# Kernel optimization log

Measured on AMD Instinct MI355X. Metric: run time of the kernel, lower is better.

Reference implementation:

```python
import jax, jax.numpy as jnp
import numpy as np

K = 3        # kernel
S = 2        # downsample scale
P = 1        # padding
C = 96       # input channels
G = C // 6   # groups = 16 (use_group=True)
BN_EPS = 1e-5


def setup_inputs() -> dict:
    key = jax.random.key(0)
    k1, k2, k3, k4, k5 = jax.random.split(key, 5)
    b, h, w = 4, 256, 512
    x = jax.random.normal(k1, (b, C, h, w), dtype=jnp.float32)
    # convbn: Conv2d(C, C*S, k=3, stride=2, pad=1, bias=False) + BatchNorm2d(C*S)
    w1 = jax.random.normal(k2, (C * S, C, K, K), dtype=jnp.float32) * 0.05
    gamma = jax.random.uniform(k3, (C * S,), dtype=jnp.float32, minval=0.5, maxval=1.5)
    beta = jax.random.normal(k4, (C * S,), dtype=jnp.float32) * 0.1
    # 1x1 conv: C*S -> G * K^2, bias=False
    w2 = jax.random.normal(k5, (G * K * K, C * S, 1, 1), dtype=jnp.float32) * 0.05
    return {"x": x, "w1": w1, "gamma": gamma, "beta": beta, "w2": w2}


def _conv(x, w, stride, pad):
    return jax.lax.conv_general_dilated(
        x, w, window_strides=(stride, stride), padding=[(pad, pad), (pad, pad)],
        dimension_numbers=("NCHW", "OIHW", "NCHW"))


def _unfold_patches(x):
    # F.unfold(x, [K,K], stride=S, padding=P) viewed as (b, c, K*K, h', w')
    b, c, h, w = x.shape
    ho, wo = h // S, w // S
    xp = jnp.pad(x, ((0, 0), (0, 0), (P, P), (P, P)))
    taps = [xp[:, :, i:i + ho * S:S, j:j + wo * S:S] for i in range(K) for j in range(K)]
    return jnp.stack(taps, axis=2)  # (b, c, K^2, h', w')


def reference(x, w1, gamma, beta, w2):
    b, c, h, w = x.shape
    ho, wo = h // S, w // S
    # conv_mask branch: conv -> BN (eval: mean=0, var=1) -> LeakyReLU(0.1) -> 1x1 conv
    y = _conv(x, w1, S, P)
    y = y * (gamma / jnp.sqrt(1.0 + BN_EPS))[None, :, None, None] + beta[None, :, None, None]
    y = jnp.where(y >= 0, y, 0.1 * y)
    mask = _conv(y, w2, 1, 0)                                  # (b, G*K^2, h', w')
    mask = mask.reshape(b, 1, G, K * K, ho, wo)
    mask = jax.nn.softmax(mask, axis=3)
    # unfold and group split: channel index = i*G + g  (torch view semantics)
    patches = _unfold_patches(x)                               # (b, c, K^2, h', w')
    patches = patches.reshape(b, c // G, G, K * K, ho, wo)
    out = jnp.sum(mask * patches, axis=3)                      # (b, c//G, G, h', w')
    return out.reshape(b, c, ho, wo)
```

## Files before the change

kernel.cpp:

```cpp
#include <hip/hip_runtime.h>
#include <hip/hip_bf16.h>

#define Bb 4
#define Cc 96
#define Hh 256
#define Ww 512
#define OC 192
#define HO 128
#define WO 256
#define Gg 16
#define CPG 6

typedef __attribute__((ext_vector_type(4))) float f32x4;
typedef __attribute__((ext_vector_type(8))) short bf16x8;
typedef __attribute__((ext_vector_type(4))) short bf16x4;

static __device__ __forceinline__ ushort f2b(float f) {
    __hip_bfloat16 h = __float2bfloat16(f);
    return *reinterpret_cast<ushort*>(&h);
}
static __device__ __forceinline__ float b2f(ushort u) {
    unsigned int v = ((unsigned int)u) << 16;
    return __builtin_bit_cast(float, v);
}

__global__ __launch_bounds__(64) void pack_w1(const float* __restrict__ w1,
                                              ushort* __restrict__ apack) {
    const int blk = blockIdx.x;
    const int k0 = blk / 12;
    const int mf = blk % 12;
    const int lane = threadIdx.x;
    const int m = mf * 16 + (lane & 15);
    const int chunk = k0 / 9;
    const int tap = k0 % 9;
    ushort* dst = apack + (((size_t)(k0 * 12 + mf) * 64) + lane) * 8;
#pragma unroll
    for (int j = 0; j < 8; ++j) {
        const int klocal = ((lane >> 4) << 3) + j;
        const int ic = chunk * 32 + klocal;
        dst[j] = f2b(w1[(size_t)(m * Cc + ic) * 9 + tap]);
    }
}

__global__ __launch_bounds__(64) void pack_w2(const float* __restrict__ w2,
                                              ushort* __restrict__ w2p) {
    const int blk = blockIdx.x;
    const int ks = blk / 9;
    const int mf = blk % 9;
    const int lane = threadIdx.x;
    const int X = lane & 15;
    const int qq = X >> 2;
    const int rr = X & 3;
    const int s = mf * 4 + rr;
    const int g = qq * 4 + s / 9;
    const int k = s % 9;
    const int m = g * 9 + k;
    ushort* dst = w2p + (((size_t)(ks * 9 + mf) * 64) + lane) * 8;
#pragma unroll
    for (int j = 0; j < 8; ++j) {
        const int klocal = ((lane >> 4) << 3) + j;
        const int c = ks * 32 + klocal;
        dst[j] = f2b(w2[(size_t)m * OC + c]);
    }
}

#define XL_MAIN (6 * 4 * 128 * 8)
#define UNION_USHORTS (XL_MAIN + 3 * 32)

__global__ __launch_bounds__(512, 4) void fused(
        const float* __restrict__ x, const ushort* __restrict__ apack,
        const ushort* __restrict__ w2p,
        const float* __restrict__ gamma, const float* __restrict__ beta,
        float* __restrict__ out) {
    __shared__ __align__(16) ushort smem[UNION_USHORTS];
    __shared__ float sc[OC], bi[OC];

    const int bid = blockIdx.x;
    const int owt = bid & 1;
    const int oh = (bid >> 1) & 127;
    const int b = bid >> 8;
    const int ow0 = owt * 128;
    const int tid = threadIdx.x;
    const int wid = tid >> 6;
    const int wm = wid & 1;
    const int wn = wid >> 1;
    const int lane = tid & 63;
    const int r = lane & 15;
    const int q = lane >> 4;

    if (tid < OC) {
        const float bnr = 1.0f / sqrtf(1.0f + 1e-5f);
        sc[tid] = gamma[tid] * bnr;
        bi[tid] = beta[tid];
    }

    f32x4 cacc[6][2];
#pragma unroll
    for (int mf = 0; mf < 6; ++mf)
#pragma unroll
        for (int nf = 0; nf < 2; ++nf) cacc[mf][nf] = (f32x4){0.f, 0.f, 0.f, 0.f};

    const size_t chs = (size_t)Hh * Ww;

    for (int chunk = 0; chunk < 3; ++chunk) {
        __syncthreads();
        const int icc = chunk * 32;
#pragma unroll
        for (int it = 0; it < 3; ++it) {
            const int g2 = tid + (it << 9);
            const int oct = g2 & 3;
            const int colp = (g2 >> 2) & 127;
            const int row = g2 >> 9;
            const int ih = 2 * oh - 1 + row;
            const int gcol = 2 * ow0 + 2 * colp;
            float2 v[8];
            if (ih >= 0) {
                const float* xp = x + ((size_t)(b * Cc + icc + (oct << 3)) * Hh + ih) * Ww + gcol;
#pragma unroll
                for (int j = 0; j < 8; ++j)
                    v[j] = *reinterpret_cast<const float2*>(xp + (size_t)j * chs);
            } else {
#pragma unroll
                for (int j = 0; j < 8; ++j) v[j] = make_float2(0.f, 0.f);
            }
            bf16x8 u0, u1;
#pragma unroll
            for (int j = 0; j < 8; ++j) {
                u0[j] = (short)f2b(v[j].x);
                u1[j] = (short)f2b(v[j].y);
            }
            *reinterpret_cast<bf16x8*>(smem + (((row * 2 + 0) * 4 + oct) * 128 + colp) * 8) = u0;
            *reinterpret_cast<bf16x8*>(smem + (((row * 2 + 1) * 4 + oct) * 128 + colp) * 8) = u1;
        }
        if (tid < 12) {
            const int oct = tid & 3;
            const int row = tid >> 2;
            const int ih = 2 * oh - 1 + row;
            const int gcol = 2 * ow0 - 1;
            float v[8];
            if (ih >= 0 && gcol >= 0) {
                const float* xp = x + ((size_t)(b * Cc + icc + (oct << 3)) * Hh + ih) * Ww + gcol;
#pragma unroll
                for (int j = 0; j < 8; ++j) v[j] = xp[(size_t)j * chs];
            } else {
#pragma unroll
                for (int j = 0; j < 8; ++j) v[j] = 0.f;
            }
            bf16x8 u;
#pragma unroll
            for (int j = 0; j < 8; ++j) u[j] = (short)f2b(v[j]);
            *reinterpret_cast<bf16x8*>(smem + XL_MAIN + row * 32 + oct * 8) = u;
        }
        __syncthreads();

#pragma unroll
        for (int tap = 0; tap < 9; ++tap) {
            const int kh = tap / 3, kw = tap % 3;
            const int par = (kw == 1) ? 0 : 1;
            const int cb = (kw == 0) ? -1 : 0;
            const int k0 = chunk * 9 + tap;

            bf16x8 af[6];
            const ushort* ap = apack + (((size_t)(k0 * 12 + wm * 6) * 64) + lane) * 8;
#pragma unroll
            for (int mf = 0; mf < 6; ++mf)
                af[mf] = *reinterpret_cast<const bf16x8*>(ap + (size_t)mf * 64 * 8);

            bf16x8 bfr[2];
#pragma unroll
            for (int nf = 0; nf < 2; ++nf) {
                const int n = wn * 32 + nf * 16 + r;
                const int colc = n + cb;
                const ushort* src = (colc >= 0)
                    ? smem + (((kh * 2 + par) * 4 + q) * 128 + colc) * 8
                    : smem + XL_MAIN + kh * 32 + q * 8;
                bfr[nf] = *reinterpret_cast<const bf16x8*>(src);
            }
#pragma unroll
            for (int mf = 0; mf < 6; ++mf)
#pragma unroll
                for (int nf = 0; nf < 2; ++nf)
                    cacc[mf][nf] = __builtin_amdgcn_mfma_f32_16x16x32_bf16(
                        af[mf], bfr[nf], cacc[mf][nf], 0, 0, 0);
        }
    }

    __syncthreads();
#pragma unroll
    for (int mf = 0; mf < 6; ++mf) {
        const int cbase = wm * 96 + mf * 16;
        const int coct = (cbase >> 3) + (q >> 1);
#pragma unroll
        for (int nf = 0; nf < 2; ++nf) {
            const int ow = wn * 32 + nf * 16 + r;
            ushort pk[4];
#pragma unroll
            for (int rr = 0; rr < 4; ++rr) {
                const int oc = cbase + q * 4 + rr;
                float v = cacc[mf][nf][rr] * sc[oc] + bi[oc];
                v = (v >= 0.f) ? v : 0.1f * v;
                pk[rr] = f2b(v);
            }
            *reinterpret_cast<bf16x4*>(smem + (coct * 128 + ow) * 8 + (q & 1) * 4) =
                *reinterpret_cast<bf16x4*>(pk);
        }
    }
    __syncthreads();

    f32x4 macc[9];
#pragma unroll
    for (int mf = 0; mf < 9; ++mf) macc[mf] = (f32x4){0.f, 0.f, 0.f, 0.f};

    const int owq = wid * 16 + r;
#pragma unroll
    for (int ks = 0; ks < 6; ++ks) {
        bf16x8 af[9];
        const ushort* ap = w2p + (((size_t)(ks * 9) * 64) + lane) * 8;
#pragma unroll
        for (int mf = 0; mf < 9; ++mf)
            af[mf] = *reinterpret_cast<const bf16x8*>(ap + (size_t)mf * 64 * 8);
        bf16x8 bfr = *reinterpret_cast<const bf16x8*>(smem + ((ks * 4 + q) * 128 + owq) * 8);
#pragma unroll
        for (int mf = 0; mf < 9; ++mf)
            macc[mf] = __builtin_amdgcn_mfma_f32_16x16x32_bf16(af[mf], bfr, macc[mf], 0, 0, 0);
    }
    __syncthreads();

    {
        const int col = (owq + q * 16) & 127;
#pragma unroll
        for (int gl = 0; gl < 4; ++gl) {
            const int g = q * 4 + gl;
            float pv[9];
            float mx = -1e30f;
#pragma unroll
            for (int k = 0; k < 9; ++k) {
                const int s = gl * 9 + k;
                pv[k] = macc[s >> 2][s & 3];
                mx = fmaxf(mx, pv[k]);
            }
            float ssum = 0.f;
#pragma unroll
            for (int k = 0; k < 9; ++k) { pv[k] = __expf(pv[k] - mx); ssum += pv[k]; }
            const float inv = 1.f / ssum;
#pragma unroll
            for (int k = 0; k < 9; ++k)
                smem[(g * 9 + k) * 128 + col] = f2b(pv[k] * inv);
        }
    }
    __syncthreads();

    const int ih0 = 2 * oh - 1;
    const bool okh0 = (oh > 0);
#pragma unroll
    for (int it = 0; it < 4; ++it) {
        const int idx = (it << 9) + tid;
        const int g = idx >> 7;
        const int owl = idx & 127;
        const int owg = ow0 + owl;
        const int rot = (g >> 2) * 16;
        const int col = (owl + rot) & 127;

        float p[9];
#pragma unroll
        for (int k = 0; k < 9; ++k) p[k] = b2f(smem[(g * 9 + k) * 128 + col]);

        const int iw0 = 2 * owg - 1;
        const bool okw0 = (owg > 0);
#pragma unroll
        for (int i = 0; i < CPG; ++i) {
            const int cc = i * Gg + g;
            const float* xc = x + (size_t)(b * Cc + cc) * chs;
            float acc = 0.f;
#pragma unroll
            for (int kh = 0; kh < 3; ++kh) {
                if (kh == 0 && !okh0) continue;
                const float* rowp = xc + (size_t)(ih0 + kh) * Ww + iw0;
                const float v0 = okw0 ? rowp[0] : 0.f;
                const float2 v12 = *reinterpret_cast<const float2*>(rowp + 1);
                acc += p[kh * 3 + 0] * v0 + p[kh * 3 + 1] * v12.x
                     + p[kh * 3 + 2] * v12.y;
            }
            out[((size_t)(b * Cc + cc) * HO + oh) * WO + owg] = acc;
        }
    }
}

extern "C" void kernel_launch(void* const* d_in, const int* in_sizes, int n_in,
                              void* d_out, int out_size, void* d_ws, size_t ws_size,
                              hipStream_t stream) {
    const float* x     = (const float*)d_in[0];
    const float* w1    = (const float*)d_in[1];
    const float* gamma = (const float*)d_in[2];
    const float* beta  = (const float*)d_in[3];
    const float* w2    = (const float*)d_in[4];
    float* out = (float*)d_out;

    ushort* apack = (ushort*)d_ws;
    ushort* w2p   = (ushort*)((char*)d_ws + 331776);

    pack_w1<<<27 * 12, 64, 0, stream>>>(w1, apack);
    pack_w2<<<6 * 9, 64, 0, stream>>>(w2, w2p);
    fused<<<Bb * HO * 2, 512, 0, stream>>>(x, apack, w2p, gamma, beta, out);
}
```

Before: 189.3 us.

## Halve output tile width per block and split mask GEMM across waves

Each block now covers 64 output columns instead of 128, so the grid doubles and shared memory per block shrinks. The launch-bounds occupancy hint rises from 4 to 8, and the block index is swizzled to change how work is ordered across the grid. In the first GEMM each wave handles one N-fragment instead of two. The 1x1-conv GEMM is split so the two wave halves compute overlapping 5-fragment M ranges, and each half then runs softmax for its own two groups. The aim is more parallelism and occupancy, at the cost of half the reuse of weight fragments per load and a tighter register budget that could cause spills.

Result: slower. 243.6 us (+28.7%).

```diff
diff --git a/kernel.cpp b/kernel.cpp
--- a/kernel.cpp
+++ b/kernel.cpp
@@ -64,10 +64,10 @@
     }
 }
 
-#define XL_MAIN (6 * 4 * 128 * 8)
+#define XL_MAIN (6 * 4 * 64 * 8)
 #define UNION_USHORTS (XL_MAIN + 3 * 32)
 
-__global__ __launch_bounds__(512, 4) void fused(
+__global__ __launch_bounds__(512, 8) void fused(
         const float* __restrict__ x, const ushort* __restrict__ apack,
         const ushort* __restrict__ w2p,
         const float* __restrict__ gamma, const float* __restrict__ beta,
@@ -75,11 +75,12 @@
     __shared__ __align__(16) ushort smem[UNION_USHORTS];
     __shared__ float sc[OC], bi[OC];
 
-    const int bid = blockIdx.x;
-    const int owt = bid & 1;
-    const int oh = (bid >> 1) & 127;
-    const int b = bid >> 8;
-    const int ow0 = owt * 128;
+    const int bid0 = blockIdx.x;
+    const int bid = (bid0 & 7) * 256 + (bid0 >> 3);
+    const int owt = bid & 3;
+    const int oh = (bid >> 2) & 127;
+    const int b = bid >> 9;
+    const int ow0 = owt * 64;
     const int tid = threadIdx.x;
     const int wid = tid >> 6;
     const int wm = wid & 1;
@@ -94,11 +95,9 @@
         bi[tid] = beta[tid];
     }
 
-    f32x4 cacc[6][2];
-#pragma unroll
-    for (int mf = 0; mf < 6; ++mf)
-#pragma unroll
-        for (int nf = 0; nf < 2; ++nf) cacc[mf][nf] = (f32x4){0.f, 0.f, 0.f, 0.f};
+    f32x4 cacc[6];
+#pragma unroll
+    for (int mf = 0; mf < 6; ++mf) cacc[mf] = (f32x4){0.f, 0.f, 0.f, 0.f};
 
     const size_t chs = (size_t)Hh * Ww;
 
@@ -106,31 +105,33 @@
         __syncthreads();
         const int icc = chunk * 32;
 #pragma unroll
-        for (int it = 0; it < 3; ++it) {
-            const int g2 = tid + (it << 9);
-            const int oct = g2 & 3;
-            const int colp = (g2 >> 2) & 127;
-            const int row = g2 >> 9;
-            const int ih = 2 * oh - 1 + row;
-            const int gcol = 2 * ow0 + 2 * colp;
-            float2 v[8];
-            if (ih >= 0) {
-                const float* xp = x + ((size_t)(b * Cc + icc + (oct << 3)) * Hh + ih) * Ww + gcol;
-#pragma unroll
-                for (int j = 0; j < 8; ++j)
-                    v[j] = *reinterpret_cast<const float2*>(xp + (size_t)j * chs);
-            } else {
-#pragma unroll
-                for (int j = 0; j < 8; ++j) v[j] = make_float2(0.f, 0.f);
-            }
-            bf16x8 u0, u1;
-#pragma unroll
-            for (int j = 0; j < 8; ++j) {
-                u0[j] = (short)f2b(v[j].x);
-                u1[j] = (short)f2b(v[j].y);
-            }
-            *reinterpret_cast<bf16x8*>(smem + (((row * 2 + 0) * 4 + oct) * 128 + colp) * 8) = u0;
-            *reinterpret_cast<bf16x8*>(smem + (((row * 2 + 1) * 4 + oct) * 128 + colp) * 8) = u1;
+        for (int it = 0; it < 2; ++it) {
+            const int g3 = (it << 9) + tid;
+            if (g3 < 768) {
+                const int oct = g3 & 3;
+                const int colp = (g3 >> 2) & 63;
+                const int row = g3 >> 8;
+                const int ih = 2 * oh - 1 + row;
+                const int gcol = 2 * (ow0 + colp);
+                float2 v[8];
+                if (ih >= 0) {
+                    const float* xp = x + ((size_t)(b * Cc + icc + (oct << 3)) * Hh + ih) * Ww + gcol;
+#pragma unroll
+                    for (int j = 0; j < 8; ++j)
+                        v[j] = *reinterpret_cast<const float2*>(xp + (size_t)j * chs);
+                } else {
+#pragma unroll
+                    for (int j = 0; j < 8; ++j) v[j] = make_float2(0.f, 0.f);
+                }
+                bf16x8 u0, u1;
+#pragma unroll
+                for (int j = 0; j < 8; ++j) {
+                    u0[j] = (short)f2b(v[j].x);
+                    u1[j] = (short)f2b(v[j].y);
+                }
+                *reinterpret_cast<bf16x8*>(smem + (((row * 2 + 0) * 4 + oct) * 64 + colp) * 8) = u0;
+                *reinterpret_cast<bf16x8*>(smem + (((row * 2 + 1) * 4 + oct) * 64 + colp) * 8) = u1;
+            }
         }
         if (tid < 12) {
             const int oct = tid & 3;
@@ -166,22 +167,15 @@
             for (int mf = 0; mf < 6; ++mf)
                 af[mf] = *reinterpret_cast<const bf16x8*>(ap + (size_t)mf * 64 * 8);
 
-            bf16x8 bfr[2];
-#pragma unroll
-            for (int nf = 0; nf < 2; ++nf) {
-                const int n = wn * 32 + nf * 16 + r;
-                const int colc = n + cb;
-                const ushort* src = (colc >= 0)
-                    ? smem + (((kh * 2 + par) * 4 + q) * 128 + colc) * 8
-                    : smem + XL_MAIN + kh * 32 + q * 8;
-                bfr[nf] = *reinterpret_cast<const bf16x8*>(src);
-            }
+            const int colc = wn * 16 + r + cb;
+            const ushort* src = (colc >= 0)
+                ? smem + (((kh * 2 + par) * 4 + q) * 64 + colc) * 8
+                : smem + XL_MAIN + kh * 32 + q * 8;
+            const bf16x8 bfr = *reinterpret_cast<const bf16x8*>(src);
 #pragma unroll
             for (int mf = 0; mf < 6; ++mf)
-#pragma unroll
-                for (int nf = 0; nf < 2; ++nf)
-                    cacc[mf][nf] = __builtin_amdgcn_mfma_f32_16x16x32_bf16(
-                        af[mf], bfr[nf], cacc[mf][nf], 0, 0, 0);
+                cacc[mf] = __builtin_amdgcn_mfma_f32_16x16x32_bf16(
+                    af[mf], bfr, cacc[mf], 0, 0, 0);
         }
     }
 
@@ -190,53 +184,53 @@
     for (int mf = 0; mf < 6; ++mf) {
         const int cbase = wm * 96 + mf * 16;
         const int coct = (cbase >> 3) + (q >> 1);
-#pragma unroll
-        for (int nf = 0; nf < 2; ++nf) {
-            const int ow = wn * 32 + nf * 16 + r;
-            ushort pk[4];
-#pragma unroll
-            for (int rr = 0; rr < 4; ++rr) {
-                const int oc = cbase + q * 4 + rr;
-                float v = cacc[mf][nf][rr] * sc[oc] + bi[oc];
-                v = (v >= 0.f) ? v : 0.1f * v;
-                pk[rr] = f2b(v);
-            }
-            *reinterpret_cast<bf16x4*>(smem + (coct * 128 + ow) * 8 + (q & 1) * 4) =
-                *reinterpret_cast<bf16x4*>(pk);
-        }
-    }
-    __syncthreads();
-
-    f32x4 macc[9];
-#pragma unroll
-    for (int mf = 0; mf < 9; ++mf) macc[mf] = (f32x4){0.f, 0.f, 0.f, 0.f};
-
-    const int owq = wid * 16 + r;
+        const int ow = wn * 16 + r;
+        ushort pk[4];
+#pragma unroll
+        for (int rr = 0; rr < 4; ++rr) {
+            const int oc = cbase + q * 4 + rr;
+            float v = cacc[mf][rr] * sc[oc] + bi[oc];
+            v = (v >= 0.f) ? v : 0.1f * v;
+            pk[rr] = f2b(v);
+        }
+        *reinterpret_cast<bf16x4*>(smem + (coct * 64 + ow) * 8 + (q & 1) * 4) =
+            *reinterpret_cast<bf16x4*>(pk);
+    }
+    __syncthreads();
+
+    const int hi = wid >> 2;
+    const int mfbase = hi * 4;
+    f32x4 macc[5];
+#pragma unroll
+    for (int mf = 0; mf < 5; ++mf) macc[mf] = (f32x4){0.f, 0.f, 0.f, 0.f};
+
+    const int owq = (wid & 3) * 16 + r;
 #pragma unroll
     for (int ks = 0; ks < 6; ++ks) {
-        bf16x8 af[9];
-        const ushort* ap = w2p + (((size_t)(ks * 9) * 64) + lane) * 8;
-#pragma unroll
-        for (int mf = 0; mf < 9; ++mf)
+        bf16x8 af[5];
+        const ushort* ap = w2p + (((size_t)(ks * 9 + mfbase) * 64) + lane) * 8;
+#pragma unroll
+        for (int mf = 0; mf < 5; ++mf)
             af[mf] = *reinterpret_cast<const bf16x8*>(ap + (size_t)mf * 64 * 8);
-        bf16x8 bfr = *reinterpret_cast<const bf16x8*>(smem + ((ks * 4 + q) * 128 + owq) * 8);
-#pragma unroll
-        for (int mf = 0; mf < 9; ++mf)
+        const bf16x8 bfr = *reinterpret_cast<const bf16x8*>(smem + ((ks * 4 + q) * 64 + owq) * 8);
+#pragma unroll
+        for (int mf = 0; mf < 5; ++mf)
             macc[mf] = __builtin_amdgcn_mfma_f32_16x16x32_bf16(af[mf], bfr, macc[mf], 0, 0, 0);
     }
     __syncthreads();
 
     {
-        const int col = (owq + q * 16) & 127;
-#pragma unroll
-        for (int gl = 0; gl < 4; ++gl) {
+        const int col = (owq + q * 16) & 63;
+#pragma unroll
+        for (int gi = 0; gi < 2; ++gi) {
+            const int gl = hi * 2 + gi;
             const int g = q * 4 + gl;
             float pv[9];
             float mx = -1e30f;
 #pragma unroll
             for (int k = 0; k < 9; ++k) {
                 const int s = gl * 9 + k;
-                pv[k] = macc[s >> 2][s & 3];
+                pv[k] = macc[(s >> 2) - mfbase][s & 3];
                 mx = fmaxf(mx, pv[k]);
             }
             float ssum = 0.f;
@@ -245,7 +239,7 @@
             const float inv = 1.f / ssum;
 #pragma unroll
             for (int k = 0; k < 9; ++k)
-                smem[(g * 9 + k) * 128 + col] = f2b(pv[k] * inv);
+                smem[(g * 9 + k) * 64 + col] = f2b(pv[k] * inv);
         }
     }
     __syncthreads();
@@ -253,17 +247,16 @@
     const int ih0 = 2 * oh - 1;
     const bool okh0 = (oh > 0);
 #pragma unroll
-    for (int it = 0; it < 4; ++it) {
+    for (int it = 0; it < 2; ++it) {
         const int idx = (it << 9) + tid;
-        const int g = idx >> 7;
-        const int owl = idx & 127;
+        const int g = idx >> 6;
+        const int owl = idx & 63;
         const int owg = ow0 + owl;
-        const int rot = (g >> 2) * 16;
-        const int col = (owl + rot) & 127;
+        const int col = (owl + (g >> 2) * 16) & 63;
 
         float p[9];
 #pragma unroll
-        for (int k = 0; k < 9; ++k) p[k] = b2f(smem[(g * 9 + k) * 128 + col]);
+        for (int k = 0; k < 9; ++k) p[k] = b2f(smem[(g * 9 + k) * 64 + col]);
 
         const int iw0 = 2 * owg - 1;
         const bool okw0 = (owg > 0);
@@ -301,5 +294,5 @@
 
     pack_w1<<<27 * 12, 64, 0, stream>>>(w1, apack);
     pack_w2<<<6 * 9, 64, 0, stream>>>(w2, w2p);
-    fused<<<Bb * HO * 2, 512, 0, stream>>>(x, apack, w2p, gamma, beta, out);
-}
+    fused<<<Bb * HO * 4, 512, 0, stream>>>(x, apack, w2p, gamma, beta, out);
+}
```
